# Kernel optimization log

Measured on AMD Instinct MI355X. Metric: run time of the kernel, lower is better.

The kernel has to match this reference:

```python
import jax, jax.numpy as jnp
import numpy as np

# dims: batch, internal ticks, neurons, input dim, NLM memory length, NLM hidden, sync pairs, out dims
B, T_TICKS, D, D_IN, M, H, P, D_OUT, D_ACT = 512, 8, 2048, 512, 16, 4, 512, 512, 512


def setup_inputs() -> dict:
    key = jax.random.key(0)
    ks = jax.random.split(key, 16)
    n = lambda k, shape: jax.random.normal(k, shape, dtype=jnp.float32)
    return {
        "x": n(ks[0], (B, D_IN)),
        # input projection
        "W_in": n(ks[1], (D_IN, D)) * 0.02,
        "b_in": jnp.zeros((D,), jnp.float32),
        # learned start post-activation state
        "z0": n(ks[2], (D,)) * 0.02,
        # synapse model: concat(z, features) -> pre-activations
        "W_syn": n(ks[3], (D + D, D)) * 0.02,
        "b_syn": jnp.zeros((D,), jnp.float32),
        # privately parameterized neuron-level models (NeuronLevelModel)
        "nlm_w1": n(ks[4], (M, H, D)) * 0.02,
        "nlm_b1": jnp.zeros((1, H, D), jnp.float32),
        "nlm_w2": n(ks[5], (H, D)) * 0.02,
        "nlm_b2": jnp.zeros((1, D), jnp.float32),
        # neural synchronization (NeuralSynchronization)
        "decay_out": jnp.zeros((P,), jnp.float32),
        "decay_action": jnp.zeros((P,), jnp.float32),
        "W_out": n(ks[6], (P, D_OUT)) * 0.02,
        "b_out": jnp.zeros((D_OUT,), jnp.float32),
        "W_act": n(ks[7], (P, D_ACT)) * 0.02,
        "b_act": jnp.zeros((D_ACT,), jnp.float32),
        # random neuron index pairs (buffers, int)
        "pairs_out": jax.random.randint(ks[8], (P, 2), 0, D),
        "pairs_action": jax.random.randint(ks[9], (P, 2), 0, D),
    }


def _nlm(hist, w1, b1, w2, b2):
    # hist: (B, D, M); private per-neuron 2-layer MLP
    h = jnp.einsum('bdM,Mhd->bdh', hist, w1) + jnp.swapaxes(b1, 1, 2)  # (B, D, H)
    h = jax.nn.relu(h)
    return jnp.einsum('bdh,hd->bd', h, w2) + b2  # (B, D)


def reference(x, W_in, b_in, z0, W_syn, b_syn, nlm_w1, nlm_b1, nlm_w2, nlm_b2,
              decay_out, decay_action, W_out, b_out, W_act, b_act,
              pairs_out, pairs_action):
    feats = x @ W_in + b_in                      # (B, D)
    z = jnp.broadcast_to(z0, (x.shape[0], D))    # (B, D)
    hist = jnp.zeros((x.shape[0], D, M), x.dtype)
    # exponential-decay sync recurrence: S_t = exp(-|r|) * S_{t-1} + z_i z_j
    # equals sum_s z_{i,s} z_{j,s} exp(-|r| (t - s))  (matches compute_sync weights)
    r_out = jnp.exp(-jnp.abs(decay_out))         # (P,)
    r_act = jnp.exp(-jnp.abs(decay_action))
    S_out = jnp.zeros((x.shape[0], P), x.dtype)
    S_act = jnp.zeros((x.shape[0], P), x.dtype)
    ys, qs = [], []
    for _ in range(T_TICKS):
        pre = jnp.concatenate([z, feats], axis=-1) @ W_syn + b_syn     # (B, D)
        hist = jnp.concatenate([hist[..., 1:], pre[..., None]], axis=-1)
        z = _nlm(hist, nlm_w1, nlm_b1, nlm_w2, nlm_b2)                 # (B, D)
        S_out = S_out * r_out + z[:, pairs_out[:, 0]] * z[:, pairs_out[:, 1]]
        S_act = S_act * r_act + z[:, pairs_action[:, 0]] * z[:, pairs_action[:, 1]]
        ys.append(S_out @ W_out + b_out)
        qs.append(S_act @ W_act + b_act)
    return jnp.stack(ys, axis=1), jnp.stack(qs, axis=1)  # (B, T, d_out), (B, T, d_action)
```

## Files before the change

### kernel.cpp

```cpp
#include <hip/hip_runtime.h>
#include <math.h>

#define Bsz 512
#define TT 8
#define Dn 2048
#define DIN 512
#define Hh 4
#define Pn 512
#define DOUT 512
#define BD (Bsz*Dn)

typedef __attribute__((ext_vector_type(8))) short s16x8;
typedef __attribute__((ext_vector_type(4))) float f32x4;
typedef __attribute__((ext_vector_type(4))) unsigned short u16x4;

__device__ __forceinline__ unsigned short f2bf(float f) {
  unsigned int u = __float_as_uint(f);
  unsigned int r = (u + 0x7fffu + ((u >> 16) & 1u)) >> 16;
  return (unsigned short)r;
}
__device__ __forceinline__ float bf2f(unsigned short h) {
  return __uint_as_float(((unsigned int)h) << 16);
}
__device__ __forceinline__ void split2(float x, unsigned short& h, unsigned short& l) {
  h = f2bf(x);
  float r = x - bf2f(h);
  l = f2bf(r);
}

#define GLOAD16(g, l) __builtin_amdgcn_global_load_lds( \
    (const __attribute__((address_space(1))) unsigned int*)(g), \
    (__attribute__((address_space(3))) unsigned int*)(l), 16, 0, 0)

__device__ __forceinline__ void gemm_core(
    const unsigned short* __restrict__ Ah, const unsigned short* __restrict__ Al,
    const unsigned short* __restrict__ BTh, const unsigned short* __restrict__ BTl,
    int K, long arow0, long brow0,
    unsigned short* LDS, f32x4 acc[2][2], int g, int qw)
{
  const int tid = threadIdx.x;
  const int lane = tid & 63;
  const int lh = lane >> 4, sc = lane & 15;
  const unsigned short* gsrc[8];
  int ldst[8];
#pragma unroll
  for (int t = 0; t < 4; ++t) {
    int rb = qw * 16 + t * 4;
    int row = rb + lh;
    int ko = ((sc & 7) ^ (row & 7)) << 3;
    gsrc[t]     = (sc >= 8 ? Al : Ah) + (size_t)(arow0 + row) * K + ko;
    ldst[t]     = rb * 128;
    gsrc[4 + t] = (sc >= 8 ? BTl : BTh) + (size_t)(brow0 + row) * K + ko;
    ldst[4 + t] = 32768 + rb * 128;
  }

  const int nI = K >> 7;

#define STAGE(ring, i_)                                              \
  {                                                                  \
    const size_t kb = ((size_t)(2 * (i_) + g)) << 6;                 \
    unsigned short* base_ = LDS + (g * 2 + (ring)) * 8192;           \
    GLOAD16(gsrc[0] + kb, base_ + ldst[0]);                          \
    GLOAD16(gsrc[1] + kb, base_ + ldst[1]);                          \
    GLOAD16(gsrc[2] + kb, base_ + ldst[2]);                          \
    GLOAD16(gsrc[3] + kb, base_ + ldst[3]);                          \
    GLOAD16(gsrc[4] + kb, base_ + ldst[4]);                          \
    GLOAD16(gsrc[5] + kb, base_ + ldst[5]);                          \
    GLOAD16(gsrc[6] + kb, base_ + ldst[6]);                          \
    GLOAD16(gsrc[7] + kb, base_ + ldst[7]);                          \
  }

  const int wm = (qw & 1) * 32, wn = (qw >> 1) * 32;
  const int lm = lane & 15, kg4 = lane >> 4;
  int aoh[2][2], boh[2][2];
#pragma unroll
  for (int u = 0; u < 2; ++u) {
    int kg = u * 4 + kg4;
#pragma unroll
    for (int mt = 0; mt < 2; ++mt) {
      int ar = wm + mt * 16 + lm;
      aoh[u][mt] = ar * 128 + ((kg ^ (ar & 7)) << 3);
    }
#pragma unroll
    for (int nt = 0; nt < 2; ++nt) {
      int br = wn + nt * 16 + lm;
      boh[u][nt] = br * 128 + ((kg ^ (br & 7)) << 3);
    }
  }

  STAGE(0, 0);
  for (int i = 0; i < nI; ++i) {
    asm volatile("s_waitcnt vmcnt(0)" ::: "memory");
    __builtin_amdgcn_s_barrier();
    if (i + 1 < nI) STAGE((i + 1) & 1, i + 1);
    const unsigned short* ab = LDS + (g * 2 + (i & 1)) * 8192;
    const unsigned short* bb = ab + 32768;
#pragma unroll
    for (int u = 0; u < 2; ++u) {
      s16x8 fah[2], fal[2], fbh[2], fbl[2];
#pragma unroll
      for (int mt = 0; mt < 2; ++mt) {
        fah[mt] = *(const s16x8*)(ab + aoh[u][mt]);
        fal[mt] = *(const s16x8*)(ab + aoh[u][mt] + 64);
      }
#pragma unroll
      for (int nt = 0; nt < 2; ++nt) {
        fbh[nt] = *(const s16x8*)(bb + boh[u][nt]);
        fbl[nt] = *(const s16x8*)(bb + boh[u][nt] + 64);
      }
      __builtin_amdgcn_s_setprio(1);
#pragma unroll
      for (int mt = 0; mt < 2; ++mt)
#pragma unroll
        for (int nt = 0; nt < 2; ++nt) {
          acc[mt][nt] = __builtin_amdgcn_mfma_f32_16x16x32_bf16(fah[mt], fbh[nt], acc[mt][nt], 0, 0, 0);
          acc[mt][nt] = __builtin_amdgcn_mfma_f32_16x16x32_bf16(fah[mt], fbl[nt], acc[mt][nt], 0, 0, 0);
          acc[mt][nt] = __builtin_amdgcn_mfma_f32_16x16x32_bf16(fal[mt], fbh[nt], acc[mt][nt], 0, 0, 0);
        }
      __builtin_amdgcn_s_setprio(0);
    }
  }
#undef STAGE

  __builtin_amdgcn_s_barrier();
  float* fred = (float*)LDS;
  const int ridx = (qw * 64 + lane) * 17;
  if (g == 1) {
#pragma unroll
    for (int mt = 0; mt < 2; ++mt)
#pragma unroll
      for (int nt = 0; nt < 2; ++nt)
#pragma unroll
        for (int r = 0; r < 4; ++r)
          fred[ridx + (mt * 2 + nt) * 4 + r] = acc[mt][nt][r];
  }
  __builtin_amdgcn_s_barrier();
  if (g == 0) {
#pragma unroll
    for (int mt = 0; mt < 2; ++mt)
#pragma unroll
      for (int nt = 0; nt < 2; ++nt)
#pragma unroll
        for (int r = 0; r < 4; ++r)
          acc[mt][nt][r] += fred[ridx + (mt * 2 + nt) * 4 + r];
  }
}

template<int MODE>
__global__ __launch_bounds__(512, 1)
void mfma_gemm(const unsigned short* __restrict__ Ah, const unsigned short* __restrict__ Al,
               const unsigned short* __restrict__ BTh, const unsigned short* __restrict__ BTl,
               const float* __restrict__ bias, float* __restrict__ Cf,
               unsigned short* __restrict__ Ch, unsigned short* __restrict__ Cl,
               int M, int N, int K, int gm, int gn)
{
  __shared__ unsigned short LDS[65536];
  int bid = blockIdx.x;
  int xcd = bid & 7, w = bid >> 3;
  int bmi = w % gm, bni = xcd * (gn >> 3) + w / gm;
  long bm = (long)bmi * 64, bn = (long)bni * 64;
  const int tid = threadIdx.x, lane = tid & 63, wave = tid >> 6;
  const int g = wave >> 2, qw = wave & 3;
  f32x4 acc[2][2];
#pragma unroll
  for (int a = 0; a < 2; ++a)
#pragma unroll
    for (int b = 0; b < 2; ++b) acc[a][b] = (f32x4)0.f;
  gemm_core(Ah, Al, BTh, BTl, K, bm, bn, LDS, acc, g, qw);
  if (g == 1) return;

  const int wm = (qw & 1) * 32, wn = (qw >> 1) * 32;
#pragma unroll
  for (int nt = 0; nt < 2; ++nt) {
    int n = (int)bn + wn + nt * 16 + (lane & 15);
    float bv = bias[n];
#pragma unroll
    for (int mt = 0; mt < 2; ++mt) {
      long r0 = bm + wm + mt * 16 + (lane >> 4) * 4;
#pragma unroll
      for (int r = 0; r < 4; ++r) {
        float v = acc[mt][nt][r] + bv;
        long R = r0 + r;
        if (MODE == 0) {
          unsigned short h_, l_; split2(v, h_, l_);
          Ch[R * N + n] = h_; Cl[R * N + n] = l_;
        } else {
          Cf[R * N + n] = v;
        }
      }
    }
  }
}

__global__ __launch_bounds__(512, 1)
void out_gemm(const unsigned short* __restrict__ S0h, const unsigned short* __restrict__ S0l,
              const unsigned short* __restrict__ S1h, const unsigned short* __restrict__ S1l,
              const unsigned short* __restrict__ W0h, const unsigned short* __restrict__ W0l,
              const unsigned short* __restrict__ W1h, const unsigned short* __restrict__ W1l,
              const float* __restrict__ bias0, const float* __restrict__ bias1,
              float* __restrict__ out0, float* __restrict__ out1)
{
  __shared__ unsigned short LDS[65536];
  const int set = blockIdx.y;
  const unsigned short* Ah = set ? S1h : S0h;
  const unsigned short* Al = set ? S1l : S0l;
  const unsigned short* BTh = set ? W1h : W0h;
  const unsigned short* BTl = set ? W1l : W0l;
  const float* bias = set ? bias1 : bias0;
  float* Cf = set ? out1 : out0;

  int bid = blockIdx.x;
  int xcd = bid & 7, w = bid >> 3;
  long bn = (long)xcd * 64;
  const int tid = threadIdx.x, lane = tid & 63, wave = tid >> 6;
  const int g = wave >> 2, qw = wave & 3;
  const int wm = (qw & 1) * 32, wn = (qw >> 1) * 32;

#pragma unroll
  for (int half = 0; half < 2; ++half) {
    long bm = (long)(w * 2 + half) * 64;
    f32x4 acc[2][2];
#pragma unroll
    for (int a = 0; a < 2; ++a)
#pragma unroll
      for (int b = 0; b < 2; ++b) acc[a][b] = (f32x4)0.f;
    gemm_core(Ah, Al, BTh, BTl, Pn, bm, bn, LDS, acc, g, qw);
    if (g == 0) {
#pragma unroll
      for (int nt = 0; nt < 2; ++nt) {
        int n = (int)bn + wn + nt * 16 + (lane & 15);
        float bv = bias[n];
#pragma unroll
        for (int mt = 0; mt < 2; ++mt) {
          long r0 = bm + wm + mt * 16 + (lane >> 4) * 4;
#pragma unroll
          for (int r = 0; r < 4; ++r) {
            float v = acc[mt][nt][r] + bv;
            long R = r0 + r;
            long t = R >> 9, b = R & 511;
            Cf[(b * TT + t) * DOUT + n] = v;
          }
        }
      }
    }
    __builtin_amdgcn_s_barrier();
  }
}

template<int TAU>
__global__ __launch_bounds__(512, 1)
void tick_mfma(const unsigned short* __restrict__ zh, const unsigned short* __restrict__ zl,
               const unsigned short* __restrict__ WTh, const unsigned short* __restrict__ WTl,
               const float* __restrict__ basep, const float* __restrict__ hist,
               float* __restrict__ histout,
               const float* __restrict__ w1, const float* __restrict__ b1,
               const float* __restrict__ w2, const float* __restrict__ b2,
               unsigned short* __restrict__ zho, unsigned short* __restrict__ zlo,
               unsigned short* __restrict__ zT)
{
  __shared__ unsigned short LDS[65536];
  int bid = blockIdx.x;
  int xcd = bid & 7, w = bid >> 3;
  int bmi = w % 8, bni = xcd * 4 + w / 8;
  long bm = (long)bmi * 64, bn = (long)bni * 64;
  const int tid = threadIdx.x, lane = tid & 63, wave = tid >> 6;
  const int g = wave >> 2, qw = wave & 3;
  f32x4 acc[2][2];
#pragma unroll
  for (int a = 0; a < 2; ++a)
#pragma unroll
    for (int b = 0; b < 2; ++b) acc[a][b] = (f32x4)0.f;
  gemm_core(zh, zl, WTh, WTl, Dn, bm, bn, LDS, acc, g, qw);
  if (g == 1) return;

  const int wm = (qw & 1) * 32, wn = (qw >> 1) * 32;
#pragma unroll
  for (int nt = 0; nt < 2; ++nt) {
    const int d = (int)bn + wn + nt * 16 + (lane & 15);
    float w2v[Hh], b1v[Hh];
#pragma unroll
    for (int hh = 0; hh < Hh; ++hh) {
      w2v[hh] = w2[hh * Dn + d];
      b1v[hh] = b1[hh * Dn + d];
    }
    const float b2v = b2[d];
#pragma unroll
    for (int mt = 0; mt < 2; ++mt) {
      const int b0 = (int)bm + wm + mt * 16 + (lane >> 4) * 4;
      float pre[4], hacc[4][Hh];
#pragma unroll
      for (int r = 0; r < 4; ++r) {
        pre[r] = acc[mt][nt][r] + basep[(size_t)(b0 + r) * Dn + d];
#pragma unroll
        for (int hh = 0; hh < Hh; ++hh) hacc[r][hh] = b1v[hh];
      }
#pragma unroll
      for (int s = 0; s < TAU; ++s) {
        float wv[Hh];
#pragma unroll
        for (int hh = 0; hh < Hh; ++hh) wv[hh] = w1[((15 - TAU + s) * Hh + hh) * Dn + d];
#pragma unroll
        for (int r = 0; r < 4; ++r) {
          float psv = hist[(size_t)s * BD + (size_t)(b0 + r) * Dn + d];
#pragma unroll
          for (int hh = 0; hh < Hh; ++hh) hacc[r][hh] = fmaf(psv, wv[hh], hacc[r][hh]);
        }
      }
      {
        float wv[Hh];
#pragma unroll
        for (int hh = 0; hh < Hh; ++hh) wv[hh] = w1[(15 * Hh + hh) * Dn + d];
#pragma unroll
        for (int r = 0; r < 4; ++r)
#pragma unroll
          for (int hh = 0; hh < Hh; ++hh) hacc[r][hh] = fmaf(pre[r], wv[hh], hacc[r][hh]);
      }
      u16x4 pack;
#pragma unroll
      for (int r = 0; r < 4; ++r) {
        histout[(size_t)(b0 + r) * Dn + d] = pre[r];
        float z = b2v;
#pragma unroll
        for (int hh = 0; hh < Hh; ++hh) z = fmaf(fmaxf(hacc[r][hh], 0.f), w2v[hh], z);
        unsigned short h_, l_; split2(z, h_, l_);
        zho[(size_t)(b0 + r) * Dn + d] = h_;
        zlo[(size_t)(b0 + r) * Dn + d] = l_;
        pack[r] = f2bf(z);
      }
      *(u16x4*)&zT[(size_t)d * Bsz + b0] = pack;
    }
  }
}

__global__ __launch_bounds__(256)
void tick0_kernel(const float* __restrict__ basep, const float* __restrict__ qpart,
                  float* __restrict__ histout,
                  const float* __restrict__ w1, const float* __restrict__ b1,
                  const float* __restrict__ w2, const float* __restrict__ b2,
                  unsigned short* __restrict__ zho, unsigned short* __restrict__ zlo,
                  unsigned short* __restrict__ zT)
{
  int g = blockIdx.x * 256 + threadIdx.x;
  int b = g >> 8;
  int d0 = (g & 255) * 8;
  float qv[8];
#pragma unroll
  for (int k = 0; k < 8; ++k) qv[k] = 0.f;
#pragma unroll
  for (int c = 0; c < 8; ++c) {
    float4 p0 = *(const float4*)(qpart + (size_t)c * Dn + d0);
    float4 p1 = *(const float4*)(qpart + (size_t)c * Dn + d0 + 4);
    qv[0] += p0.x; qv[1] += p0.y; qv[2] += p0.z; qv[3] += p0.w;
    qv[4] += p1.x; qv[5] += p1.y; qv[6] += p1.z; qv[7] += p1.w;
  }
#pragma unroll
  for (int k = 0; k < 8; ++k) {
    int d = d0 + k;
    float pre = basep[(size_t)b * Dn + d] + qv[k];
    histout[(size_t)b * Dn + d] = pre;
    float z = b2[d];
#pragma unroll
    for (int hh = 0; hh < Hh; ++hh) {
      float h = fmaf(pre, w1[(15 * Hh + hh) * Dn + d], b1[hh * Dn + d]);
      z = fmaf(fmaxf(h, 0.f), w2[hh * Dn + d], z);
    }
    unsigned short h_, l_; split2(z, h_, l_);
    zho[(size_t)b * Dn + d] = h_;
    zlo[(size_t)b * Dn + d] = l_;
    zT[(size_t)d * Bsz + b] = f2bf(z);
  }
}

__global__ __launch_bounds__(512)
void sync_kernel(const unsigned short* __restrict__ zT,
                 const int* __restrict__ pairs0, const int* __restrict__ pairs1,
                 const float* __restrict__ decay0, const float* __restrict__ decay1,
                 unsigned short* __restrict__ Sh0, unsigned short* __restrict__ Sl0,
                 unsigned short* __restrict__ Sh1, unsigned short* __restrict__ Sl1)
{
  __shared__ float Ls[8][8][65];
  const int set = blockIdx.y;
  const int* pairs = set ? pairs1 : pairs0;
  const float* decay = set ? decay1 : decay0;
  unsigned short* Sh = set ? Sh1 : Sh0;
  unsigned short* Sl = set ? Sl1 : Sl0;
  const int tid = threadIdx.x;
  const int lb = tid & 63, pl = tid >> 6;
  const int p = blockIdx.x * 8 + pl;
  const int i = pairs[2 * p], j = pairs[2 * p + 1];
  const float r = expf(-fabsf(decay[p]));
  const int pb = tid & 7, bb2 = tid >> 3;
  for (int bb = 0; bb < 8; ++bb) {
    int b = bb * 64 + lb;
    float S = 0.f, St[8];
#pragma unroll
    for (int t = 0; t < 8; ++t) {
      float zi = bf2f(zT[(size_t)t * BD + (size_t)i * Bsz + b]);
      float zj = bf2f(zT[(size_t)t * BD + (size_t)j * Bsz + b]);
      S = fmaf(S, r, zi * zj);
      St[t] = S;
    }
#pragma unroll
    for (int t = 0; t < 8; ++t) Ls[pl][t][lb] = St[t];
    __syncthreads();
#pragma unroll
    for (int t = 0; t < 8; ++t) {
      float v = Ls[pb][t][bb2];
      unsigned short h_, l_; split2(v, h_, l_);
      size_t off = ((size_t)t * Bsz + bb * 64 + bb2) * Pn + blockIdx.x * 8 + pb;
      Sh[off] = h_; Sl[off] = l_;
    }
    __syncthreads();
  }
}

__device__ __forceinline__ void transpose_tile(const float* __restrict__ in, int ldin,
    unsigned short* __restrict__ Th, unsigned short* __restrict__ Tl, int K,
    int kb, int nb, float T[64][65])
{
  int k0 = kb * 64, n0 = nb * 64;
  int tid = threadIdx.x;
  int r = tid >> 2, c0 = (tid & 3) * 16;
#pragma unroll
  for (int cc = 0; cc < 16; cc += 4) {
    float4 v = *(const float4*)(in + (size_t)(k0 + r) * ldin + n0 + c0 + cc);
    T[c0 + cc + 0][r] = v.x; T[c0 + cc + 1][r] = v.y;
    T[c0 + cc + 2][r] = v.z; T[c0 + cc + 3][r] = v.w;
  }
  __syncthreads();
  int n = tid >> 2, kc = (tid & 3) * 16;
#pragma unroll
  for (int kk = 0; kk < 16; ++kk) {
    float v = T[n][kc + kk];
    unsigned short h_, l_; split2(v, h_, l_);
    Th[(size_t)(n0 + n) * K + k0 + kc + kk] = h_;
    Tl[(size_t)(n0 + n) * K + k0 + kc + kk] = l_;
  }
}

__global__ __launch_bounds__(256)
void prep_kernel(const float* __restrict__ W_syn, const float* __restrict__ W_in,
                 const float* __restrict__ W_out, const float* __restrict__ W_act,
                 const float* __restrict__ x, const float* __restrict__ z0,
                 unsigned short* WtTh, unsigned short* WtTl,
                 unsigned short* WbTh, unsigned short* WbTl,
                 unsigned short* WinTh, unsigned short* WinTl,
                 unsigned short* WoTh, unsigned short* WoTl,
                 unsigned short* WaTh, unsigned short* WaTl,
                 unsigned short* xh, unsigned short* xl,
                 float* qpart)
{
  __shared__ float T[64][65];
  const int b = blockIdx.x;
  const int tid = threadIdx.x;
  if (b < 1024) {
    transpose_tile(W_syn, Dn, WtTh, WtTl, Dn, b & 31, b >> 5, T);
  } else if (b < 2048) {
    int b2 = b - 1024;
    transpose_tile(W_syn + (size_t)Dn * Dn, Dn, WbTh, WbTl, Dn, b2 & 31, b2 >> 5, T);
  } else if (b < 2304) {
    int b2 = b - 2048;
    transpose_tile(W_in, Dn, WinTh, WinTl, DIN, b2 & 7, b2 >> 3, T);
  } else if (b < 2368) {
    int b2 = b - 2304;
    transpose_tile(W_out, DOUT, WoTh, WoTl, Pn, b2 & 7, b2 >> 3, T);
  } else if (b < 2432) {
    int b2 = b - 2368;
    transpose_tile(W_act, DOUT, WaTh, WaTl, Pn, b2 & 7, b2 >> 3, T);
  } else if (b < 2688) {
    int i = (b - 2432) * 256 + tid;
    float4 v = *(const float4*)(x + (size_t)i * 4);
    u16x4 h, l;
    unsigned short th, tl;
    split2(v.x, th, tl); h[0] = th; l[0] = tl;
    split2(v.y, th, tl); h[1] = th; l[1] = tl;
    split2(v.z, th, tl); h[2] = th; l[2] = tl;
    split2(v.w, th, tl); h[3] = th; l[3] = tl;
    *(u16x4*)(xh + (size_t)i * 4) = h;
    *(u16x4*)(xl + (size_t)i * 4) = l;
  } else {
    int idx = b - 2688;
    int colb = idx & 31, kc = idx >> 5;
    float (*red)[64] = (float(*)[64])T;
    const int c = tid & 63, strip = tid >> 6;
    const int col = colb * 64 + c;
    const int k0 = (kc * 4 + strip) * 64;
    float acc = 0.f;
#pragma unroll 8
    for (int k = k0; k < k0 + 64; ++k)
      acc = fmaf(z0[k], W_syn[(size_t)k * Dn + col], acc);
    red[strip][c] = acc;
    __syncthreads();
    if (strip == 0)
      qpart[(size_t)kc * Dn + col] = red[0][c] + red[1][c] + red[2][c] + red[3][c];
  }
}

extern "C" void kernel_launch(void* const* d_in, const int* in_sizes, int n_in,
                              void* d_out, int out_size, void* d_ws, size_t ws_size,
                              hipStream_t stream) {
  const float* x      = (const float*)d_in[0];
  const float* W_in   = (const float*)d_in[1];
  const float* b_in   = (const float*)d_in[2];
  const float* z0     = (const float*)d_in[3];
  const float* W_syn  = (const float*)d_in[4];
  const float* b_syn  = (const float*)d_in[5];
  const float* w1     = (const float*)d_in[6];
  const float* b1     = (const float*)d_in[7];
  const float* w2     = (const float*)d_in[8];
  const float* b2     = (const float*)d_in[9];
  const float* decay_out = (const float*)d_in[10];
  const float* decay_act = (const float*)d_in[11];
  const float* W_out  = (const float*)d_in[12];
  const float* b_out  = (const float*)d_in[13];
  const float* W_act  = (const float*)d_in[14];
  const float* b_act  = (const float*)d_in[15];
  const int* pairs_out = (const int*)d_in[16];
  const int* pairs_act = (const int*)d_in[17];

  char* W = (char*)d_ws;
  auto alloc = [&](size_t bytes) { char* p = W; W += (bytes + 255) & ~255ull; return p; };
  unsigned short* WtTh = (unsigned short*)alloc((size_t)Dn * Dn * 2);
  unsigned short* WtTl = (unsigned short*)alloc((size_t)Dn * Dn * 2);
  unsigned short* WbTh = (unsigned short*)alloc((size_t)Dn * Dn * 2);
  unsigned short* WbTl = (unsigned short*)alloc((size_t)Dn * Dn * 2);
  unsigned short* WinTh = (unsigned short*)alloc((size_t)Dn * DIN * 2);
  unsigned short* WinTl = (unsigned short*)alloc((size_t)Dn * DIN * 2);
  unsigned short* WoTh = (unsigned short*)alloc((size_t)DOUT * Pn * 2);
  unsigned short* WoTl = (unsigned short*)alloc((size_t)DOUT * Pn * 2);
  unsigned short* WaTh = (unsigned short*)alloc((size_t)DOUT * Pn * 2);
  unsigned short* WaTl = (unsigned short*)alloc((size_t)DOUT * Pn * 2);
  unsigned short* xh = (unsigned short*)alloc((size_t)Bsz * DIN * 2);
  unsigned short* xl = (unsigned short*)alloc((size_t)Bsz * DIN * 2);
  unsigned short* fh = (unsigned short*)alloc((size_t)BD * 2);
  unsigned short* fl = (unsigned short*)alloc((size_t)BD * 2);
  float* qpart = (float*)alloc(8 * Dn * 4);
  float* base  = (float*)alloc((size_t)BD * 4);
  float* hist  = (float*)alloc((size_t)TT * BD * 4);
  unsigned short* zbh[2], *zbl[2];
  zbh[0] = (unsigned short*)alloc((size_t)BD * 2);
  zbl[0] = (unsigned short*)alloc((size_t)BD * 2);
  zbh[1] = (unsigned short*)alloc((size_t)BD * 2);
  zbl[1] = (unsigned short*)alloc((size_t)BD * 2);
  unsigned short* zT = (unsigned short*)alloc((size_t)TT * BD * 2);
  unsigned short* Sh0 = WbTh;
  unsigned short* Sl0 = WbTh + (size_t)TT * Bsz * Pn;
  unsigned short* Sh1 = WbTl;
  unsigned short* Sl1 = WbTl + (size_t)TT * Bsz * Pn;

  float* outy = (float*)d_out;
  float* outq = outy + (size_t)Bsz * TT * DOUT;

  dim3 blk(256);
  dim3 blk512(512);
  prep_kernel<<<dim3(2944), blk, 0, stream>>>(
      W_syn, W_in, W_out, W_act, x, z0,
      WtTh, WtTl, WbTh, WbTl, WinTh, WinTl, WoTh, WoTl, WaTh, WaTl,
      xh, xl, qpart);
  mfma_gemm<0><<<dim3(256), blk512, 0, stream>>>(xh, xl, WinTh, WinTl, b_in, nullptr, fh, fl,
                                                 Bsz, Dn, DIN, 8, 32);
  mfma_gemm<1><<<dim3(256), blk512, 0, stream>>>(fh, fl, WbTh, WbTl, b_syn, base, nullptr, nullptr,
                                                 Bsz, Dn, Dn, 8, 32);
  tick0_kernel<<<dim3(512), blk, 0, stream>>>(base, qpart, hist, w1, b1, w2, b2,
                                              zbh[0], zbl[0], zT);
  for (int tau = 1; tau < TT; ++tau) {
    const unsigned short* zih = zbh[(tau + 1) & 1];
    const unsigned short* zil = zbl[(tau + 1) & 1];
    unsigned short* zoh = zbh[tau & 1];
    unsigned short* zol = zbl[tau & 1];
    float* ho = hist + (size_t)tau * BD;
    unsigned short* zTo = zT + (size_t)tau * BD;
    switch (tau) {
      case 1: tick_mfma<1><<<dim3(256), blk512, 0, stream>>>(zih, zil, WtTh, WtTl, base, hist, ho, w1, b1, w2, b2, zoh, zol, zTo); break;
      case 2: tick_mfma<2><<<dim3(256), blk512, 0, stream>>>(zih, zil, WtTh, WtTl, base, hist, ho, w1, b1, w2, b2, zoh, zol, zTo); break;
      case 3: tick_mfma<3><<<dim3(256), blk512, 0, stream>>>(zih, zil, WtTh, WtTl, base, hist, ho, w1, b1, w2, b2, zoh, zol, zTo); break;
      case 4: tick_mfma<4><<<dim3(256), blk512, 0, stream>>>(zih, zil, WtTh, WtTl, base, hist, ho, w1, b1, w2, b2, zoh, zol, zTo); break;
      case 5: tick_mfma<5><<<dim3(256), blk512, 0, stream>>>(zih, zil, WtTh, WtTl, base, hist, ho, w1, b1, w2, b2, zoh, zol, zTo); break;
      case 6: tick_mfma<6><<<dim3(256), blk512, 0, stream>>>(zih, zil, WtTh, WtTl, base, hist, ho, w1, b1, w2, b2, zoh, zol, zTo); break;
      case 7: tick_mfma<7><<<dim3(256), blk512, 0, stream>>>(zih, zil, WtTh, WtTl, base, hist, ho, w1, b1, w2, b2, zoh, zol, zTo); break;
    }
  }
  sync_kernel<<<dim3(Pn / 8, 2), dim3(512), 0, stream>>>(zT, pairs_out, pairs_act,
                                                         decay_out, decay_act,
                                                         Sh0, Sl0, Sh1, Sl1);
  out_gemm<<<dim3(256, 2), blk512, 0, stream>>>(Sh0, Sl0, Sh1, Sl1,
                                                WoTh, WoTl, WaTh, WaTl,
                                                b_out, b_act, outy, outq);
}
```

Baseline: 283.4 us.

## Restructure GEMM core into triple-buffered pipeline with split-K across wave groups

The GEMM core now has the two wave groups split the loads of each stage: one group fetches the A tile and the other the B tile. Each stage covers a 64-wide K slab, and the groups split the K halves inside it for MFMA. A three-slot LDS ring with a prefetch distance of two replaces the double buffer, and the wait becomes vmcnt(4) instead of draining all loads. The aim is to overlap global-to-LDS loads with MFMA work and to issue fewer loads per thread per stage. In exchange there are twice as many iterations and barriers, and LDS use drops to 96KB.

```diff
diff --git a/kernel.cpp b/kernel.cpp
--- a/kernel.cpp
+++ b/kernel.cpp
@@ -41,84 +41,80 @@
   const int tid = threadIdx.x;
   const int lane = tid & 63;
   const int lh = lane >> 4, sc = lane & 15;
-  const unsigned short* gsrc[8];
-  int ldst[8];
+  const unsigned short* Xh = g ? BTh : Ah;
+  const unsigned short* Xl = g ? BTl : Al;
+  const long row0 = g ? brow0 : arow0;
+  const int bofs = g ? 8192 : 0;
+  const unsigned short* gsrc[4];
+  int ldst[4];
 #pragma unroll
   for (int t = 0; t < 4; ++t) {
     int rb = qw * 16 + t * 4;
     int row = rb + lh;
     int ko = ((sc & 7) ^ (row & 7)) << 3;
-    gsrc[t]     = (sc >= 8 ? Al : Ah) + (size_t)(arow0 + row) * K + ko;
-    ldst[t]     = rb * 128;
-    gsrc[4 + t] = (sc >= 8 ? BTl : BTh) + (size_t)(brow0 + row) * K + ko;
-    ldst[4 + t] = 32768 + rb * 128;
-  }
-
-  const int nI = K >> 7;
-
-#define STAGE(ring, i_)                                              \
+    gsrc[t] = (sc >= 8 ? Xl : Xh) + (size_t)(row0 + row) * K + ko;
+    ldst[t] = bofs + rb * 128;
+  }
+
+  const int nI = K >> 6;
+
+#define STAGE(slot, i_)                                              \
   {                                                                  \
-    const size_t kb = ((size_t)(2 * (i_) + g)) << 6;                 \
-    unsigned short* base_ = LDS + (g * 2 + (ring)) * 8192;           \
+    const size_t kb = (size_t)(i_) * 64;                             \
+    unsigned short* base_ = LDS + (slot) * 16384;                    \
     GLOAD16(gsrc[0] + kb, base_ + ldst[0]);                          \
     GLOAD16(gsrc[1] + kb, base_ + ldst[1]);                          \
     GLOAD16(gsrc[2] + kb, base_ + ldst[2]);                          \
     GLOAD16(gsrc[3] + kb, base_ + ldst[3]);                          \
-    GLOAD16(gsrc[4] + kb, base_ + ldst[4]);                          \
-    GLOAD16(gsrc[5] + kb, base_ + ldst[5]);                          \
-    GLOAD16(gsrc[6] + kb, base_ + ldst[6]);                          \
-    GLOAD16(gsrc[7] + kb, base_ + ldst[7]);                          \
   }
 
   const int wm = (qw & 1) * 32, wn = (qw >> 1) * 32;
   const int lm = lane & 15, kg4 = lane >> 4;
-  int aoh[2][2], boh[2][2];
-#pragma unroll
-  for (int u = 0; u < 2; ++u) {
-    int kg = u * 4 + kg4;
+  const int kg = g * 4 + kg4;
+  int aoh[2], boh[2];
+#pragma unroll
+  for (int mt = 0; mt < 2; ++mt) {
+    int ar = wm + mt * 16 + lm;
+    aoh[mt] = ar * 128 + ((kg ^ (ar & 7)) << 3);
+  }
+#pragma unroll
+  for (int nt = 0; nt < 2; ++nt) {
+    int br = wn + nt * 16 + lm;
+    boh[nt] = 8192 + br * 128 + ((kg ^ (br & 7)) << 3);
+  }
+
+  STAGE(0, 0);
+  STAGE(1, 1);
+  int slot = 0, nslot = 2;
+  for (int i = 0; i < nI; ++i) {
+    if (i < nI - 1) asm volatile("s_waitcnt vmcnt(4)" ::: "memory");
+    else            asm volatile("s_waitcnt vmcnt(0)" ::: "memory");
+    __builtin_amdgcn_s_barrier();
+    if (i + 2 < nI) STAGE(nslot, i + 2);
+    const unsigned short* ab = LDS + slot * 16384;
+    s16x8 fah[2], fal[2], fbh[2], fbl[2];
 #pragma unroll
     for (int mt = 0; mt < 2; ++mt) {
-      int ar = wm + mt * 16 + lm;
-      aoh[u][mt] = ar * 128 + ((kg ^ (ar & 7)) << 3);
+      fah[mt] = *(const s16x8*)(ab + aoh[mt]);
+      fal[mt] = *(const s16x8*)(ab + aoh[mt] + 64);
     }
 #pragma unroll
     for (int nt = 0; nt < 2; ++nt) {
-      int br = wn + nt * 16 + lm;
-      boh[u][nt] = br * 128 + ((kg ^ (br & 7)) << 3);
-    }
-  }
-
-  STAGE(0, 0);
-  for (int i = 0; i < nI; ++i) {
-    asm volatile("s_waitcnt vmcnt(0)" ::: "memory");
-    __builtin_amdgcn_s_barrier();
-    if (i + 1 < nI) STAGE((i + 1) & 1, i + 1);
-    const unsigned short* ab = LDS + (g * 2 + (i & 1)) * 8192;
-    const unsigned short* bb = ab + 32768;
-#pragma unroll
-    for (int u = 0; u < 2; ++u) {
-      s16x8 fah[2], fal[2], fbh[2], fbl[2];
-#pragma unroll
-      for (int mt = 0; mt < 2; ++mt) {
-        fah[mt] = *(const s16x8*)(ab + aoh[u][mt]);
-        fal[mt] = *(const s16x8*)(ab + aoh[u][mt] + 64);
-      }
+      fbh[nt] = *(const s16x8*)(ab + boh[nt]);
+      fbl[nt] = *(const s16x8*)(ab + boh[nt] + 64);
+    }
+    __builtin_amdgcn_s_setprio(1);
+#pragma unroll
+    for (int mt = 0; mt < 2; ++mt)
 #pragma unroll
       for (int nt = 0; nt < 2; ++nt) {
-        fbh[nt] = *(const s16x8*)(bb + boh[u][nt]);
-        fbl[nt] = *(const s16x8*)(bb + boh[u][nt] + 64);
-      }
-      __builtin_amdgcn_s_setprio(1);
-#pragma unroll
-      for (int mt = 0; mt < 2; ++mt)
-#pragma unroll
-        for (int nt = 0; nt < 2; ++nt) {
-          acc[mt][nt] = __builtin_amdgcn_mfma_f32_16x16x32_bf16(fah[mt], fbh[nt], acc[mt][nt], 0, 0, 0);
-          acc[mt][nt] = __builtin_amdgcn_mfma_f32_16x16x32_bf16(fah[mt], fbl[nt], acc[mt][nt], 0, 0, 0);
-          acc[mt][nt] = __builtin_amdgcn_mfma_f32_16x16x32_bf16(fal[mt], fbh[nt], acc[mt][nt], 0, 0, 0);
-        }
-      __builtin_amdgcn_s_setprio(0);
-    }
+        acc[mt][nt] = __builtin_amdgcn_mfma_f32_16x16x32_bf16(fah[mt], fbh[nt], acc[mt][nt], 0, 0, 0);
+        acc[mt][nt] = __builtin_amdgcn_mfma_f32_16x16x32_bf16(fah[mt], fbl[nt], acc[mt][nt], 0, 0, 0);
+        acc[mt][nt] = __builtin_amdgcn_mfma_f32_16x16x32_bf16(fal[mt], fbh[nt], acc[mt][nt], 0, 0, 0);
+      }
+    __builtin_amdgcn_s_setprio(0);
+    slot = (slot == 2) ? 0 : slot + 1;
+    nslot = (nslot == 2) ? 0 : nslot + 1;
   }
 #undef STAGE
 
@@ -154,7 +150,7 @@
                unsigned short* __restrict__ Ch, unsigned short* __restrict__ Cl,
                int M, int N, int K, int gm, int gn)
 {
-  __shared__ unsigned short LDS[65536];
+  __shared__ unsigned short LDS[49152];
   int bid = blockIdx.x;
   int xcd = bid & 7, w = bid >> 3;
   int bmi = w % gm, bni = xcd * (gn >> 3) + w / gm;
@@ -200,7 +196,7 @@
               const float* __restrict__ bias0, const float* __restrict__ bias1,
               float* __restrict__ out0, float* __restrict__ out1)
 {
-  __shared__ unsigned short LDS[65536];
+  __shared__ unsigned short LDS[49152];
   const int set = blockIdx.y;
   const unsigned short* Ah = set ? S1h : S0h;
   const unsigned short* Al = set ? S1l : S0l;
@@ -258,7 +254,7 @@
                unsigned short* __restrict__ zho, unsigned short* __restrict__ zlo,
                unsigned short* __restrict__ zT)
 {
-  __shared__ unsigned short LDS[65536];
+  __shared__ unsigned short LDS[49152];
   int bid = blockIdx.x;
   int xcd = bid & 7, w = bid >> 3;
   int bmi = w % 8, bni = xcd * 4 + w / 8;
```

Measured after the change: 278.2 us. Within noise of the previous version (-1.8%).
